# Kernel optimization log

Hardware: AMD Instinct MI355X
Metric: run time of the kernel (lower is better)

## Reference

```python
import jax, jax.numpy as jnp
import numpy as np

B, N, D = 2, 1024, 1024
H = 4
KD = 512          # key_dim = d_model * 0.5
VD = 1024         # value_dim = d_model
DK = KD // H      # 128 head_qk_dim
DV = VD // H      # 256 head_v_dim
LR = 16           # gate_low_rank_dim
GLN = 16.0        # gate_logit_normalizer
EPS = 1e-5


def setup_inputs() -> dict:
    key = jax.random.key(0)
    ks = jax.random.split(key, 10)
    s = 0.02
    return {
        "x": jax.random.normal(ks[0], (B, N, D), jnp.float32),
        "Wq": jax.random.normal(ks[1], (D, KD), jnp.float32) * s,
        "Wk": jax.random.normal(ks[2], (D, KD), jnp.float32) * s,
        "Wv": jax.random.normal(ks[3], (D, VD), jnp.float32) * s,
        "Wg": jax.random.normal(ks[4], (D, VD), jnp.float32) * s,
        "Wgk1": jax.random.normal(ks[5], (D, LR), jnp.float32) * s,
        "Wgk2": jax.random.normal(ks[6], (LR, KD), jnp.float32) * s,
        "bgk2": jax.random.normal(ks[7], (KD,), jnp.float32) * s,
        "Wout": jax.random.normal(ks[8], (VD, D), jnp.float32) * s,
        "rms_w": jnp.ones((DV,), jnp.float32),
    }


def _split_heads(t, h):
    b, n, hd = t.shape
    return t.reshape(b, n, h, hd // h).transpose(0, 2, 1, 3)  # b h n d


def _gla_scan(q, k, v, g):
    # q,k: [b,h,n,dk]; v: [b,h,n,dv]; g: [b,h,n,dk] (log-decay)
    b, h, n, dk = q.shape
    dv = v.shape[-1]
    qT = jnp.moveaxis(q, 2, 0)  # [n,b,h,dk]
    kT = jnp.moveaxis(k, 2, 0)
    vT = jnp.moveaxis(v, 2, 0)
    gT = jnp.moveaxis(g, 2, 0)

    def step(S, inp):
        qt, kt, vt, gt = inp
        # S_t = diag(exp(g_t)) S_{t-1} + k_t v_t^T ; o_t = q_t S_t
        S = S * jnp.exp(gt)[..., None] + kt[..., None] * vt[..., None, :]
        ot = jnp.einsum('bhk,bhkv->bhv', qt, S)
        return S, ot

    S0 = jnp.zeros((b, h, dk, dv), q.dtype)
    _, o = jax.lax.scan(step, S0, (qT, kT, vT, gT))
    return jnp.moveaxis(o, 0, 2)  # [b,h,n,dv]


def reference(x, Wq, Wk, Wv, Wg, Wgk1, Wgk2, bgk2, Wout, rms_w):
    q = _split_heads(x @ Wq, H)
    k = _split_heads(x @ Wk, H)
    v = _split_heads(x @ Wv, H)
    g = jax.nn.log_sigmoid((x @ Wgk1) @ Wgk2 + bgk2) / GLN
    g = jnp.maximum(g, -3.0)  # chunk mode clamp
    g = _split_heads(g, H)
    o = _gla_scan(q, k, v, g)               # [b,h,n,dv]
    o = o.transpose(0, 2, 1, 3)             # [b,n,h,dv]
    # RMSNorm over head_v_dim
    o = o * jax.lax.rsqrt(jnp.mean(o * o, axis=-1, keepdims=True) + EPS) * rms_w
    o = o.reshape(o.shape[0], o.shape[1], VD)
    o = o * jax.nn.silu(x @ Wg)
    return o @ Wout
```

## Files before the change

kernel.cpp:

```cpp
#include <hip/hip_runtime.h>
#include <math.h>


typedef __attribute__((ext_vector_type(4))) float vf4;
typedef __attribute__((ext_vector_type(4))) unsigned int vu4;
typedef __attribute__((ext_vector_type(8))) short short8;

#define DEVI static __device__ __forceinline__
DEVI vf4 vzero() { vf4 x = {0.f, 0.f, 0.f, 0.f}; return x; }

DEVI float bf2f(unsigned int u) {
  union { unsigned int i; float f; } c; c.i = u << 16; return c.f;
}
DEVI unsigned short f2bf(float f) {
  union { float f; unsigned int i; } c; c.f = f;
  unsigned int i = c.i;
  return (unsigned short)((i + 0x7fffu + ((i >> 16) & 1u)) >> 16);
}
DEVI void unpack8(vu4 r, float* f) {
  f[0] = bf2f(r.x & 0xffffu); f[1] = bf2f(r.x >> 16);
  f[2] = bf2f(r.y & 0xffffu); f[3] = bf2f(r.y >> 16);
  f[4] = bf2f(r.z & 0xffffu); f[5] = bf2f(r.z >> 16);
  f[6] = bf2f(r.w & 0xffffu); f[7] = bf2f(r.w >> 16);
}
DEVI vu4 pack8(const float* f) {
  vu4 o;
  o.x = (unsigned int)f2bf(f[0]) | ((unsigned int)f2bf(f[1]) << 16);
  o.y = (unsigned int)f2bf(f[2]) | ((unsigned int)f2bf(f[3]) << 16);
  o.z = (unsigned int)f2bf(f[4]) | ((unsigned int)f2bf(f[5]) << 16);
  o.w = (unsigned int)f2bf(f[6]) | ((unsigned int)f2bf(f[7]) << 16);
  return o;
}

DEVI void gld16(const unsigned short* g, unsigned short* l) {
  __builtin_amdgcn_global_load_lds(
      (const __attribute__((address_space(1))) unsigned int*)g,
      (__attribute__((address_space(3))) unsigned int*)l,
      16, 0, 0);
}

__global__ __launch_bounds__(256)
void prep_k(const float* __restrict__ Wq, const float* __restrict__ Wk,
            const float* __restrict__ Wv, const float* __restrict__ Wg,
            const float* __restrict__ Wo, const float* __restrict__ X,
            unsigned short* __restrict__ wqT, unsigned short* __restrict__ wkT,
            unsigned short* __restrict__ wvT, unsigned short* __restrict__ wgT,
            unsigned short* __restrict__ woT, unsigned short* __restrict__ xb) {
  __shared__ float T[64][65];
  const int ct = blockIdx.x, kt = blockIdx.y;
  const int t = threadIdx.x;
  const int r = t >> 2, s = t & 3;
  if (ct >= 64) {
    const int rt = ct - 64;
    const size_t base = (size_t)(rt * 64 + r) * 1024 + kt * 64 + s * 16;
    float f[16];
    *(vf4*)&f[0]  = *(const vf4*)(X + base);
    *(vf4*)&f[4]  = *(const vf4*)(X + base + 4);
    *(vf4*)&f[8]  = *(const vf4*)(X + base + 8);
    *(vf4*)&f[12] = *(const vf4*)(X + base + 12);
    *(vu4*)(xb + base) = pack8(f);
    *(vu4*)(xb + base + 8) = pack8(f + 8);
    return;
  }
  const float* W; unsigned short* O; int N; int cb;
  if (ct < 8)       { W = Wq; O = wqT; N = 512;  cb = ct; }
  else if (ct < 16) { W = Wk; O = wkT; N = 512;  cb = ct - 8; }
  else if (ct < 32) { W = Wv; O = wvT; N = 1024; cb = ct - 16; }
  else if (ct < 48) { W = Wg; O = wgT; N = 1024; cb = ct - 32; }
  else              { W = Wo; O = woT; N = 1024; cb = ct - 48; }
  const float* src = W + (size_t)(kt * 64 + r) * N + cb * 64 + s * 16;
#pragma unroll
  for (int u = 0; u < 4; ++u) {
    vf4 v4 = *(const vf4*)(src + u * 4);
    T[r][s * 16 + u * 4 + 0] = v4.x;
    T[r][s * 16 + u * 4 + 1] = v4.y;
    T[r][s * 16 + u * 4 + 2] = v4.z;
    T[r][s * 16 + u * 4 + 3] = v4.w;
  }
  __syncthreads();
  unsigned int pk[8];
#pragma unroll
  for (int u = 0; u < 8; ++u) {
    unsigned int lo = f2bf(T[s * 16 + 2 * u][r]);
    unsigned int hi = f2bf(T[s * 16 + 2 * u + 1][r]);
    pk[u] = lo | (hi << 16);
  }
  unsigned short* dst = O + (size_t)(cb * 64 + r) * 1024 + kt * 64 + s * 16;
  *(vu4*)dst = *(vu4*)&pk[0];
  *(vu4*)(dst + 8) = *(vu4*)&pk[4];
}

__global__ __launch_bounds__(256)
void proj_mfma_k(const unsigned short* __restrict__ xb,
                 const unsigned short* __restrict__ wqT, const unsigned short* __restrict__ wkT,
                 const unsigned short* __restrict__ wvT, const unsigned short* __restrict__ wgT,
                 unsigned short* __restrict__ qb, unsigned short* __restrict__ kb,
                 unsigned short* __restrict__ vb, unsigned short* __restrict__ sgb) {
  __shared__ __align__(16) unsigned short As[128 * 64];
  __shared__ __align__(16) unsigned short Bs[128 * 64];
  const int t = threadIdx.x;
  const int m0 = blockIdx.y << 7;
  const int nt = blockIdx.x;
  const unsigned short* WT; int n0; int kind;
  if (nt < 4)       { WT = wqT; n0 = nt << 7;        kind = 0; }
  else if (nt < 8)  { WT = wkT; n0 = (nt - 4) << 7;  kind = 1; }
  else if (nt < 16) { WT = wvT; n0 = (nt - 8) << 7;  kind = 2; }
  else              { WT = wgT; n0 = (nt - 16) << 7; kind = 3; }

  const int w = t >> 6, lane = t & 63;
  const int wm = (w >> 1) << 6, wn = (w & 1) << 6;
  const int qd = lane >> 4, m = lane & 15;
  const int srow = lane >> 3;
  const int scol = ((lane & 7) ^ srow) << 3;

  vf4 acc[4][4];
#pragma unroll
  for (int i = 0; i < 4; ++i)
#pragma unroll
    for (int j = 0; j < 4; ++j) acc[i][j] = vzero();

  for (int k0 = 0; k0 < 1024; k0 += 64) {
    __syncthreads();
#pragma unroll
    for (int cc = 0; cc < 4; ++cc) {
      const int c = (w << 2) + cc;
      const int row = (c << 3) + srow;
      gld16(xb + (size_t)(m0 + row) * 1024 + k0 + scol, (unsigned short*)As + (c << 9));
      gld16(WT + (size_t)(n0 + row) * 1024 + k0 + scol, (unsigned short*)Bs + (c << 9));
    }
    __syncthreads();
#pragma unroll
    for (int ks = 0; ks < 2; ++ks) {
      const int sw = (((ks << 2) + qd) ^ (m & 7)) << 3;
      short8 af[4], bf[4];
#pragma unroll
      for (int i = 0; i < 4; ++i)
        af[i] = *(const short8*)&As[(wm + i * 16 + m) * 64 + sw];
#pragma unroll
      for (int j = 0; j < 4; ++j)
        bf[j] = *(const short8*)&Bs[(wn + j * 16 + m) * 64 + sw];
#pragma unroll
      for (int i = 0; i < 4; ++i)
#pragma unroll
        for (int j = 0; j < 4; ++j)
          acc[i][j] = __builtin_amdgcn_mfma_f32_16x16x32_bf16(af[i], bf[j], acc[i][j], 0, 0, 0);
    }
  }
#pragma unroll
  for (int i = 0; i < 4; ++i) {
#pragma unroll
    for (int j = 0; j < 4; ++j) {
#pragma unroll
      for (int r = 0; r < 4; ++r) {
        const int grow = m0 + wm + i * 16 + qd * 4 + r;
        const int gcol = n0 + wn + j * 16 + m;
        float val = acc[i][j][r];
        if (kind == 0)      qb[(size_t)grow * 512 + gcol] = f2bf(val);
        else if (kind == 1) kb[(size_t)grow * 512 + gcol] = f2bf(val);
        else if (kind == 2) vb[(size_t)grow * 1024 + gcol] = f2bf(val);
        else {
          val = val / (1.f + expf(-val));
          sgb[(size_t)grow * 1024 + gcol] = f2bf(val);
        }
      }
    }
  }
}

__global__ __launch_bounds__(256)
void out_mfma_k(const unsigned short* __restrict__ Ab,
                const unsigned short* __restrict__ woT, float* __restrict__ Y) {
  __shared__ __align__(16) unsigned short As[64 * 64];
  __shared__ __align__(16) unsigned short Bs[128 * 64];
  const int t = threadIdx.x;
  const int m0 = blockIdx.y << 6;
  const int n0 = blockIdx.x << 7;
  const int w = t >> 6, lane = t & 63;
  const int wm = (w >> 1) * 32, wn = (w & 1) * 64;
  const int qd = lane >> 4, m = lane & 15;
  const int srow = lane >> 3;
  const int scol = ((lane & 7) ^ srow) << 3;

  vf4 acc[2][4];
#pragma unroll
  for (int i = 0; i < 2; ++i)
#pragma unroll
    for (int j = 0; j < 4; ++j) acc[i][j] = vzero();

  for (int k0 = 0; k0 < 1024; k0 += 64) {
    __syncthreads();
#pragma unroll
    for (int cc = 0; cc < 2; ++cc) {
      const int c = (w << 1) + cc;
      const int row = (c << 3) + srow;
      gld16(Ab + (size_t)(m0 + row) * 1024 + k0 + scol, (unsigned short*)As + (c << 9));
    }
#pragma unroll
    for (int cc = 0; cc < 4; ++cc) {
      const int c = (w << 2) + cc;
      const int row = (c << 3) + srow;
      gld16(woT + (size_t)(n0 + row) * 1024 + k0 + scol, (unsigned short*)Bs + (c << 9));
    }
    __syncthreads();
#pragma unroll
    for (int ks = 0; ks < 2; ++ks) {
      const int sw = (((ks << 2) + qd) ^ (m & 7)) << 3;
      short8 af[2], bf[4];
#pragma unroll
      for (int i = 0; i < 2; ++i)
        af[i] = *(const short8*)&As[(wm + i * 16 + m) * 64 + sw];
#pragma unroll
      for (int j = 0; j < 4; ++j)
        bf[j] = *(const short8*)&Bs[(wn + j * 16 + m) * 64 + sw];
#pragma unroll
      for (int i = 0; i < 2; ++i)
#pragma unroll
        for (int j = 0; j < 4; ++j)
          acc[i][j] = __builtin_amdgcn_mfma_f32_16x16x32_bf16(af[i], bf[j], acc[i][j], 0, 0, 0);
    }
  }
#pragma unroll
  for (int i = 0; i < 2; ++i)
#pragma unroll
    for (int j = 0; j < 4; ++j)
#pragma unroll
      for (int r = 0; r < 4; ++r) {
        const int grow = m0 + wm + i * 16 + qd * 4 + r;
        const int gcol = n0 + wn + j * 16 + m;
        Y[(size_t)grow * 1024 + gcol] = acc[i][j][r];
      }
}

__global__ __launch_bounds__(64)
void lowrank_k(const float* __restrict__ X, const float* __restrict__ W1,
               float* __restrict__ xl) {
  const int row = blockIdx.x;
  const int t = threadIdx.x;
  float acc[16];
#pragma unroll
  for (int c2 = 0; c2 < 16; ++c2) acc[c2] = 0.f;
  const float* xp = X + (size_t)row * 1024 + t * 16;
  float xv[16];
#pragma unroll
  for (int u = 0; u < 4; ++u)
    *(vf4*)&xv[u * 4] = *(const vf4*)(xp + u * 4);
#pragma unroll
  for (int j = 0; j < 16; ++j) {
    const float* wp = W1 + (size_t)(t * 16 + j) * 16;
    float wv[16];
#pragma unroll
    for (int u = 0; u < 4; ++u)
      *(vf4*)&wv[u * 4] = *(const vf4*)(wp + u * 4);
#pragma unroll
    for (int c2 = 0; c2 < 16; ++c2) acc[c2] = fmaf(xv[j], wv[c2], acc[c2]);
  }
#pragma unroll
  for (int mm = 1; mm < 64; mm <<= 1) {
#pragma unroll
    for (int c2 = 0; c2 < 16; ++c2) acc[c2] += __shfl_xor(acc[c2], mm, 64);
  }
  if (t == 0) {
#pragma unroll
    for (int c2 = 0; c2 < 16; ++c2) xl[(size_t)row * 16 + c2] = acc[c2];
  }
}

__global__ __launch_bounds__(256)
void gate_scan_k(const float* __restrict__ xl, const float* __restrict__ W2,
                 const float* __restrict__ bias,
                 unsigned short* __restrict__ q, unsigned short* __restrict__ k,
                 float* __restrict__ ebtot) {
  const int t = threadIdx.x;
  const int w = t >> 6, lane = t & 63;
  const int wid = blockIdx.x * 4 + w;
  const int kt = wid & 31;
  const int c = (wid >> 5) & 15;
  const int b = wid >> 9;
  const int kbase = kt * 16;
  const size_t rowbase = (size_t)b * 1024 + c * 64;

  const float* xp = xl + (rowbase + lane) * 16;
  float xv[16];
#pragma unroll
  for (int u = 0; u < 4; ++u)
    *(vf4*)&xv[u * 4] = *(const vf4*)(xp + u * 4);

  const size_t a = (rowbase + lane) * 512 + kbase;
  vu4 qr0 = *(const vu4*)(q + a), qr1 = *(const vu4*)(q + a + 8);
  vu4 kr0 = *(const vu4*)(k + a), kr1 = *(const vu4*)(k + a + 8);
  float qf[16], kf[16];
  unpack8(qr0, qf); unpack8(qr1, qf + 8);
  unpack8(kr0, kf); unpack8(kr1, kf + 8);

  float gf[16];
#pragma unroll
  for (int cc = 0; cc < 16; ++cc) {
    const int col = kbase + cc;
    float z = bias[col];
#pragma unroll
    for (int j = 0; j < 16; ++j) z = fmaf(xv[j], W2[j * 512 + col], z);
    float ls = fminf(z, 0.f) - log1pf(expf(-fabsf(z)));
    float g = fmaxf(ls * (1.f / 16.f), -3.f);
#pragma unroll
    for (int d = 1; d < 64; d <<= 1) {
      float up = __shfl_up(g, d, 64);
      if (lane >= d) g += up;
    }
    qf[cc] *= expf(g);
    kf[cc] *= expf(fminf(-g, 80.f));
    gf[cc] = g;
  }
  *(vu4*)(q + a) = pack8(qf);
  *(vu4*)(q + a + 8) = pack8(qf + 8);
  *(vu4*)(k + a) = pack8(kf);
  *(vu4*)(k + a + 8) = pack8(kf + 8);
  if (lane == 63) {
    float* ep = ebtot + ((size_t)b * 16 + c) * 512 + kbase;
#pragma unroll
    for (int cc = 0; cc < 16; ++cc) ep[cc] = expf(gf[cc]);
  }
}

__global__ __launch_bounds__(256)
void intra_kv_k(const unsigned short* __restrict__ q16, const unsigned short* __restrict__ k16,
                const unsigned short* __restrict__ v, float* __restrict__ o,
                unsigned short* __restrict__ ST) {
  __shared__ __align__(16) unsigned short Qs[64 * 136];
  __shared__ __align__(16) unsigned short Ks[64 * 136];
  __shared__ __align__(16) unsigned short Kt[128 * 68];
  __shared__ __align__(16) unsigned short Vt[128 * 68];
  __shared__ __align__(16) unsigned short Asb[64 * 68];
  const int t = threadIdx.x;
  const int vh = blockIdx.x, c = blockIdx.y, bh = blockIdx.z;
  const int b = bh >> 2, h = bh & 3;
  const size_t rowbase = (size_t)b * 1024 + c * 64;

#pragma unroll
  for (int u2 = 0; u2 < 4; ++u2) {
    const int id = t + (u2 << 8);
    const int row = id >> 4, kg = id & 15;
    vu4 rq = *(const vu4*)(q16 + (rowbase + row) * 512 + h * 128 + kg * 8);
    *(vu4*)&Qs[row * 136 + kg * 8] = rq;
    vu4 rk = *(const vu4*)(k16 + (rowbase + row) * 512 + h * 128 + kg * 8);
    *(vu4*)&Ks[row * 136 + kg * 8] = rk;
    const unsigned short* kp = (const unsigned short*)&rk;
#pragma unroll
    for (int u = 0; u < 8; ++u)
      Kt[(kg * 8 + u) * 68 + row] = kp[u];
    vu4 rv = *(const vu4*)(v + (rowbase + row) * 1024 + h * 256 + vh * 128 + kg * 8);
    const unsigned short* vp = (const unsigned short*)&rv;
#pragma unroll
    for (int u = 0; u < 8; ++u)
      Vt[(kg * 8 + u) * 68 + row] = vp[u];
  }
  __syncthreads();

  const int w = t >> 6, lane = t & 63;
  const int qd = lane >> 4, m = lane & 15;

  {
    short8 af[4];
#pragma unroll
    for (int kf = 0; kf < 4; ++kf)
      af[kf] = *(const short8*)&Qs[(w * 16 + m) * 136 + kf * 32 + qd * 8];
    vf4 acc[4];
#pragma unroll
    for (int jt = 0; jt < 4; ++jt) acc[jt] = vzero();
#pragma unroll
    for (int jt = 0; jt < 4; ++jt)
#pragma unroll
      for (int kf = 0; kf < 4; ++kf) {
        short8 bfr = *(const short8*)&Ks[(jt * 16 + m) * 136 + kf * 32 + qd * 8];
        acc[jt] = __builtin_amdgcn_mfma_f32_16x16x32_bf16(af[kf], bfr, acc[jt], 0, 0, 0);
      }
#pragma unroll
    for (int jt = 0; jt < 4; ++jt)
#pragma unroll
      for (int r = 0; r < 4; ++r) {
        const int i = w * 16 + qd * 4 + r;
        const int j = jt * 16 + m;
        Asb[i * 68 + j] = f2bf((j <= i) ? acc[jt][r] : 0.f);
      }
  }
  __syncthreads();

  {
    vf4 acc2[4][2];
#pragma unroll
    for (int mt = 0; mt < 4; ++mt) { acc2[mt][0] = vzero(); acc2[mt][1] = vzero(); }
#pragma unroll
    for (int kf = 0; kf < 2; ++kf) {
      short8 bf0 = *(const short8*)&Vt[(w * 32 + m) * 68 + kf * 32 + qd * 8];
      short8 bf1 = *(const short8*)&Vt[(w * 32 + 16 + m) * 68 + kf * 32 + qd * 8];
#pragma unroll
      for (int mt = 0; mt < 4; ++mt) {
        short8 af = *(const short8*)&Asb[(mt * 16 + m) * 68 + kf * 32 + qd * 8];
        acc2[mt][0] = __builtin_amdgcn_mfma_f32_16x16x32_bf16(af, bf0, acc2[mt][0], 0, 0, 0);
        acc2[mt][1] = __builtin_amdgcn_mfma_f32_16x16x32_bf16(af, bf1, acc2[mt][1], 0, 0, 0);
      }
    }
#pragma unroll
    for (int mt = 0; mt < 4; ++mt)
#pragma unroll
      for (int nt = 0; nt < 2; ++nt)
#pragma unroll
        for (int r = 0; r < 4; ++r) {
          const int i = mt * 16 + qd * 4 + r;
          const int vc = h * 256 + vh * 128 + w * 32 + nt * 16 + m;
          o[(rowbase + i) * 1024 + vc] = acc2[mt][nt][r];
        }
  }

  {
    short8 af3[2][2];
#pragma unroll
    for (int mt = 0; mt < 2; ++mt)
#pragma unroll
      for (int kf = 0; kf < 2; ++kf)
        af3[mt][kf] = *(const short8*)&Vt[(w * 32 + mt * 16 + m) * 68 + kf * 32 + qd * 8];
#pragma unroll
    for (int nt = 0; nt < 8; ++nt) {
      vf4 a0 = vzero(), a1 = vzero();
#pragma unroll
      for (int kf = 0; kf < 2; ++kf) {
        short8 bfr = *(const short8*)&Kt[(nt * 16 + m) * 68 + kf * 32 + qd * 8];
        a0 = __builtin_amdgcn_mfma_f32_16x16x32_bf16(af3[0][kf], bfr, a0, 0, 0, 0);
        a1 = __builtin_amdgcn_mfma_f32_16x16x32_bf16(af3[1][kf], bfr, a1, 0, 0, 0);
      }
      const size_t sbase = (size_t)(bh * 16 + c) * 256 + vh * 128 + w * 32;
#pragma unroll
      for (int r = 0; r < 4; ++r) {
        ST[(sbase + qd * 4 + r) * 128 + nt * 16 + m] = f2bf(a0[r]);
        ST[(sbase + 16 + qd * 4 + r) * 128 + nt * 16 + m] = f2bf(a1[r]);
      }
    }
  }
}

__global__ __launch_bounds__(256)
void state_scan_k(unsigned short* __restrict__ ST, const float* __restrict__ ebtot) {
  const int idx = blockIdx.x * 256 + threadIdx.x;
  const int kg = idx & 15;
  const int vv = (idx >> 4) & 255;
  const int bh = idx >> 12;
  const int b = bh >> 2, h = bh & 3;
  float s[8];
#pragma unroll
  for (int u = 0; u < 8; ++u) s[u] = 0.f;
  for (int c = 0; c < 16; ++c) {
    unsigned short* p = ST + ((size_t)(bh * 16 + c) * 256 + vv) * 128 + kg * 8;
    const float* ep = ebtot + ((size_t)b * 16 + c) * 512 + h * 128 + kg * 8;
    float e[8];
    *(vf4*)&e[0] = *(const vf4*)ep;
    *(vf4*)&e[4] = *(const vf4*)(ep + 4);
    float kv[8];
    unpack8(*(const vu4*)p, kv);
    *(vu4*)p = pack8(s);
#pragma unroll
    for (int u = 0; u < 8; ++u) s[u] = (s[u] + kv[u]) * e[u];
  }
}

__global__ __launch_bounds__(256)
void o_inter_k(const unsigned short* __restrict__ q16, const unsigned short* __restrict__ ST,
               float* __restrict__ o) {
  __shared__ __align__(16) unsigned short Qs[64 * 136];
  __shared__ __align__(16) unsigned short Ss[128 * 136];
  const int t = threadIdx.x;
  const int vt = blockIdx.x, c = blockIdx.y, bh = blockIdx.z;
  const int b = bh >> 2, h = bh & 3;
  const size_t rowbase = (size_t)b * 1024 + c * 64;

#pragma unroll
  for (int u2 = 0; u2 < 4; ++u2) {
    const int id = t + (u2 << 8);
    const int row = id >> 4, kg = id & 15;
    *(vu4*)&Qs[row * 136 + kg * 8] =
        *(const vu4*)(q16 + (rowbase + row) * 512 + h * 128 + kg * 8);
  }
#pragma unroll
  for (int u2 = 0; u2 < 8; ++u2) {
    const int id = t + (u2 << 8);
    const int vrow = id >> 4, kg = id & 15;
    *(vu4*)&Ss[vrow * 136 + kg * 8] =
        *(const vu4*)(ST + ((size_t)(bh * 16 + c) * 256 + vt * 128 + vrow) * 128 + kg * 8);
  }
  __syncthreads();

  const int w = t >> 6, lane = t & 63;
  const int qd = lane >> 4, m = lane & 15;
  short8 af[4];
#pragma unroll
  for (int kf = 0; kf < 4; ++kf)
    af[kf] = *(const short8*)&Qs[(w * 16 + m) * 136 + kf * 32 + qd * 8];
#pragma unroll
  for (int nt = 0; nt < 8; ++nt) {
    vf4 acc = vzero();
#pragma unroll
    for (int kf = 0; kf < 4; ++kf) {
      short8 bfr = *(const short8*)&Ss[(nt * 16 + m) * 136 + kf * 32 + qd * 8];
      acc = __builtin_amdgcn_mfma_f32_16x16x32_bf16(af[kf], bfr, acc, 0, 0, 0);
    }
    float* base = o + (rowbase + w * 16 + qd * 4) * 1024 + h * 256 + vt * 128 + nt * 16 + m;
#pragma unroll
    for (int r = 0; r < 4; ++r)
      base[(size_t)r * 1024] += acc[r];
  }
}

__global__ __launch_bounds__(256)
void norm_gate_k(const float* __restrict__ o, const float* __restrict__ rmsw,
                 const unsigned short* __restrict__ sg,
                 unsigned short* __restrict__ ob) {
  __shared__ float red[4];
  const int grp = blockIdx.x;
  const int row = grp >> 2, h = grp & 3;
  const int t = threadIdx.x;
  const size_t idx = (size_t)row * 1024 + h * 256 + t;
  const float val = o[idx];
  float ss = val * val;
#pragma unroll
  for (int mm = 1; mm < 64; mm <<= 1) ss += __shfl_xor(ss, mm, 64);
  if ((t & 63) == 0) red[t >> 6] = ss;
  __syncthreads();
  const float tot = red[0] + red[1] + red[2] + red[3];
  const float scale = rsqrtf(tot * (1.f / 256.f) + 1e-5f);
  ob[idx] = f2bf(val * scale * rmsw[t] * bf2f((unsigned int)sg[idx]));
}

extern "C" void kernel_launch(void* const* d_in, const int* in_sizes, int n_in,
                              void* d_out, int out_size, void* d_ws, size_t ws_size,
                              hipStream_t stream) {
  const float* x    = (const float*)d_in[0];
  const float* Wq   = (const float*)d_in[1];
  const float* Wk   = (const float*)d_in[2];
  const float* Wv   = (const float*)d_in[3];
  const float* Wg   = (const float*)d_in[4];
  const float* Wgk1 = (const float*)d_in[5];
  const float* Wgk2 = (const float*)d_in[6];
  const float* bgk2 = (const float*)d_in[7];
  const float* Wout = (const float*)d_in[8];
  const float* rmsw = (const float*)d_in[9];

  const size_t MB = 1u << 20;
  char* w = (char*)d_ws;
  unsigned short* qb16   = (unsigned short*)(w);
  unsigned short* kb16   = (unsigned short*)(w + 2 * MB);
  unsigned short* vbuf   = (unsigned short*)(w + 4 * MB);
  unsigned short* sgbuf  = (unsigned short*)(w + 8 * MB);
  float*          obuf   = (float*)(w + 12 * MB);
  char*           sreg   = w + 20 * MB;
  unsigned short* xb     = (unsigned short*)sreg;
  unsigned short* STbuf  = (unsigned short*)sreg;
  unsigned short* obuf_b = (unsigned short*)sreg;
  float*          xlbuf  = (float*)(w + 28 * MB);
  float*          ebbuf  = (float*)(w + 28 * MB + 131072);
  unsigned short* wqT    = (unsigned short*)(w + 29 * MB);
  unsigned short* wkT    = (unsigned short*)(w + 30 * MB);
  unsigned short* wvT    = (unsigned short*)(w + 31 * MB);
  unsigned short* wgT    = (unsigned short*)(w + 33 * MB);
  unsigned short* woT    = (unsigned short*)(w + 35 * MB);

  prep_k<<<dim3(96, 16), 256, 0, stream>>>(Wq, Wk, Wv, Wg, Wout, x,
                                           wqT, wkT, wvT, wgT, woT, xb);
  lowrank_k<<<2048, 64, 0, stream>>>(x, Wgk1, xlbuf);
  proj_mfma_k<<<dim3(24, 16), 256, 0, stream>>>(xb, wqT, wkT, wvT, wgT, qb16, kb16, vbuf, sgbuf);
  gate_scan_k<<<256, 256, 0, stream>>>(xlbuf, Wgk2, bgk2, qb16, kb16, ebbuf);
  intra_kv_k<<<dim3(2, 16, 8), 256, 0, stream>>>(qb16, kb16, vbuf, obuf, STbuf);
  state_scan_k<<<128, 256, 0, stream>>>(STbuf, ebbuf);
  o_inter_k<<<dim3(2, 16, 8), 256, 0, stream>>>(qb16, STbuf, obuf);
  norm_gate_k<<<8192, 256, 0, stream>>>(obuf, rmsw, sgbuf, obuf_b);
  out_mfma_k<<<dim3(8, 32), 256, 0, stream>>>(obuf_b, woT, (float*)d_out);
}
```

Measured before the change: 194.2 us.

## Fuse gate computation into intra/inter chunk kernels and merge prep with lowrank

Removes the separate gate_scan kernel by recomputing the log-decay cumsum inside both the intra-chunk and inter-chunk kernels, applying the decay scaling to q/k in shared memory instead of writing them back to global memory. The lowrank projection is folded into the prep kernel as extra blocks, and norm_gate is vectorised with one wave per head row. This cuts two launches and a global read-modify-write of q and k, at the cost of redundant gate computation in each block and more shared memory (EQ/EK arrays), which may lower occupancy.

```diff
diff --git a/kernel.cpp b/kernel.cpp
--- a/kernel.cpp
+++ b/kernel.cpp
@@ -5,6 +5,7 @@
 typedef __attribute__((ext_vector_type(4))) float vf4;
 typedef __attribute__((ext_vector_type(4))) unsigned int vu4;
 typedef __attribute__((ext_vector_type(8))) short short8;
+typedef __attribute__((ext_vector_type(4))) unsigned short us4;
 
 #define DEVI static __device__ __forceinline__
 DEVI vf4 vzero() { vf4 x = {0.f, 0.f, 0.f, 0.f}; return x; }
@@ -40,15 +41,52 @@
 }
 
 __global__ __launch_bounds__(256)
-void prep_k(const float* __restrict__ Wq, const float* __restrict__ Wk,
-            const float* __restrict__ Wv, const float* __restrict__ Wg,
-            const float* __restrict__ Wo, const float* __restrict__ X,
-            unsigned short* __restrict__ wqT, unsigned short* __restrict__ wkT,
-            unsigned short* __restrict__ wvT, unsigned short* __restrict__ wgT,
-            unsigned short* __restrict__ woT, unsigned short* __restrict__ xb) {
+void prep_lowrank_k(const float* __restrict__ Wq, const float* __restrict__ Wk,
+                    const float* __restrict__ Wv, const float* __restrict__ Wg,
+                    const float* __restrict__ Wo, const float* __restrict__ X,
+                    const float* __restrict__ Wgk1,
+                    unsigned short* __restrict__ wqT, unsigned short* __restrict__ wkT,
+                    unsigned short* __restrict__ wvT, unsigned short* __restrict__ wgT,
+                    unsigned short* __restrict__ woT, unsigned short* __restrict__ xb,
+                    float* __restrict__ xl) {
   __shared__ float T[64][65];
-  const int ct = blockIdx.x, kt = blockIdx.y;
+  const int bid = blockIdx.x;
   const int t = threadIdx.x;
+
+  if (bid >= 1536) {
+    const int w = t >> 6, lane = t & 63;
+    const int row = (bid - 1536) * 4 + w;
+    float acc[16];
+#pragma unroll
+    for (int c2 = 0; c2 < 16; ++c2) acc[c2] = 0.f;
+    const float* xp = X + (size_t)row * 1024 + lane * 16;
+    float xv[16];
+#pragma unroll
+    for (int u = 0; u < 4; ++u)
+      *(vf4*)&xv[u * 4] = *(const vf4*)(xp + u * 4);
+#pragma unroll
+    for (int j = 0; j < 16; ++j) {
+      const float* wp = Wgk1 + (size_t)(lane * 16 + j) * 16;
+      float wv[16];
+#pragma unroll
+      for (int u = 0; u < 4; ++u)
+        *(vf4*)&wv[u * 4] = *(const vf4*)(wp + u * 4);
+#pragma unroll
+      for (int c2 = 0; c2 < 16; ++c2) acc[c2] = fmaf(xv[j], wv[c2], acc[c2]);
+    }
+#pragma unroll
+    for (int mm = 1; mm < 64; mm <<= 1) {
+#pragma unroll
+      for (int c2 = 0; c2 < 16; ++c2) acc[c2] += __shfl_xor(acc[c2], mm, 64);
+    }
+    if (lane == 0) {
+#pragma unroll
+      for (int c2 = 0; c2 < 16; ++c2) xl[(size_t)row * 16 + c2] = acc[c2];
+    }
+    return;
+  }
+
+  const int ct = bid % 96, kt = bid / 96;
   const int r = t >> 2, s = t & 3;
   if (ct >= 64) {
     const int rt = ct - 64;
@@ -168,6 +206,288 @@
 }
 
 __global__ __launch_bounds__(256)
+void intra_gate_k(const float* __restrict__ xl, const float* __restrict__ W2,
+                  const float* __restrict__ bias,
+                  const unsigned short* __restrict__ q16, const unsigned short* __restrict__ k16,
+                  const unsigned short* __restrict__ v, float* __restrict__ o,
+                  unsigned short* __restrict__ ST, float* __restrict__ ebtot) {
+  __shared__ __align__(16) unsigned short Qs[64 * 136];
+  __shared__ __align__(16) unsigned short Ks[64 * 136];
+  __shared__ __align__(16) unsigned short Kt[128 * 68];
+  __shared__ __align__(16) unsigned short Vt[128 * 68];
+  __shared__ __align__(16) unsigned short Asb[64 * 68];
+  __shared__ float EQ[128 * 65];
+  __shared__ float EK[128 * 65];
+  const int t = threadIdx.x;
+  const int vh = blockIdx.x, c = blockIdx.y, bh = blockIdx.z;
+  const int b = bh >> 2, h = bh & 3;
+  const size_t rowbase = (size_t)b * 1024 + c * 64;
+  const int w = t >> 6, lane = t & 63;
+  const int qd = lane >> 4, m = lane & 15;
+
+  {
+    const float* xp = xl + (rowbase + lane) * 16;
+    float xv[16];
+#pragma unroll
+    for (int u = 0; u < 4; ++u)
+      *(vf4*)&xv[u * 4] = *(const vf4*)(xp + u * 4);
+#pragma unroll
+    for (int cc = 0; cc < 32; ++cc) {
+      const int cl = w * 32 + cc;
+      const int col = h * 128 + cl;
+      float z = bias[col];
+#pragma unroll
+      for (int j = 0; j < 16; ++j) z = fmaf(xv[j], W2[j * 512 + col], z);
+      float ls = fminf(z, 0.f) - log1pf(expf(-fabsf(z)));
+      float g = fmaxf(ls * (1.f / 16.f), -3.f);
+#pragma unroll
+      for (int d = 1; d < 64; d <<= 1) {
+        float up = __shfl_up(g, d, 64);
+        if (lane >= d) g += up;
+      }
+      EQ[cl * 65 + lane] = expf(g);
+      EK[cl * 65 + lane] = expf(fminf(-g, 80.f));
+      if (vh == 0 && lane == 63)
+        ebtot[((size_t)b * 16 + c) * 512 + col] = expf(g);
+    }
+  }
+  __syncthreads();
+
+#pragma unroll
+  for (int u2 = 0; u2 < 4; ++u2) {
+    const int id = t + (u2 << 8);
+    const int row = id >> 4, kg = id & 15;
+    vu4 rq = *(const vu4*)(q16 + (rowbase + row) * 512 + h * 128 + kg * 8);
+    vu4 rk = *(const vu4*)(k16 + (rowbase + row) * 512 + h * 128 + kg * 8);
+    float qf[8], kf[8];
+    unpack8(rq, qf); unpack8(rk, kf);
+#pragma unroll
+    for (int u = 0; u < 8; ++u) {
+      qf[u] *= EQ[(kg * 8 + u) * 65 + row];
+      kf[u] *= EK[(kg * 8 + u) * 65 + row];
+    }
+    vu4 pq = pack8(qf), pk4 = pack8(kf);
+    *(vu4*)&Qs[row * 136 + kg * 8] = pq;
+    *(vu4*)&Ks[row * 136 + kg * 8] = pk4;
+    const unsigned short* kp = (const unsigned short*)&pk4;
+#pragma unroll
+    for (int u = 0; u < 8; ++u)
+      Kt[(kg * 8 + u) * 68 + row] = kp[u];
+    vu4 rv = *(const vu4*)(v + (rowbase + row) * 1024 + h * 256 + vh * 128 + kg * 8);
+    const unsigned short* vp = (const unsigned short*)&rv;
+#pragma unroll
+    for (int u = 0; u < 8; ++u)
+      Vt[(kg * 8 + u) * 68 + row] = vp[u];
+  }
+  __syncthreads();
+
+  {
+    short8 af[4];
+#pragma unroll
+    for (int kf = 0; kf < 4; ++kf)
+      af[kf] = *(const short8*)&Qs[(w * 16 + m) * 136 + kf * 32 + qd * 8];
+    vf4 acc[4];
+#pragma unroll
+    for (int jt = 0; jt < 4; ++jt) acc[jt] = vzero();
+#pragma unroll
+    for (int jt = 0; jt < 4; ++jt)
+#pragma unroll
+      for (int kf = 0; kf < 4; ++kf) {
+        short8 bfr = *(const short8*)&Ks[(jt * 16 + m) * 136 + kf * 32 + qd * 8];
+        acc[jt] = __builtin_amdgcn_mfma_f32_16x16x32_bf16(af[kf], bfr, acc[jt], 0, 0, 0);
+      }
+#pragma unroll
+    for (int jt = 0; jt < 4; ++jt)
+#pragma unroll
+      for (int r = 0; r < 4; ++r) {
+        const int i = w * 16 + qd * 4 + r;
+        const int j = jt * 16 + m;
+        Asb[i * 68 + j] = f2bf((j <= i) ? acc[jt][r] : 0.f);
+      }
+  }
+  __syncthreads();
+
+  {
+    vf4 acc2[4][2];
+#pragma unroll
+    for (int mt = 0; mt < 4; ++mt) { acc2[mt][0] = vzero(); acc2[mt][1] = vzero(); }
+#pragma unroll
+    for (int kf = 0; kf < 2; ++kf) {
+      short8 bf0 = *(const short8*)&Vt[(w * 32 + m) * 68 + kf * 32 + qd * 8];
+      short8 bf1 = *(const short8*)&Vt[(w * 32 + 16 + m) * 68 + kf * 32 + qd * 8];
+#pragma unroll
+      for (int mt = 0; mt < 4; ++mt) {
+        short8 af = *(const short8*)&Asb[(mt * 16 + m) * 68 + kf * 32 + qd * 8];
+        acc2[mt][0] = __builtin_amdgcn_mfma_f32_16x16x32_bf16(af, bf0, acc2[mt][0], 0, 0, 0);
+        acc2[mt][1] = __builtin_amdgcn_mfma_f32_16x16x32_bf16(af, bf1, acc2[mt][1], 0, 0, 0);
+      }
+    }
+#pragma unroll
+    for (int mt = 0; mt < 4; ++mt)
+#pragma unroll
+      for (int nt = 0; nt < 2; ++nt)
+#pragma unroll
+        for (int r = 0; r < 4; ++r) {
+          const int i = mt * 16 + qd * 4 + r;
+          const int vc = h * 256 + vh * 128 + w * 32 + nt * 16 + m;
+          o[(rowbase + i) * 1024 + vc] = acc2[mt][nt][r];
+        }
+  }
+
+  {
+    short8 af3[2][2];
+#pragma unroll
+    for (int mt = 0; mt < 2; ++mt)
+#pragma unroll
+      for (int kf = 0; kf < 2; ++kf)
+        af3[mt][kf] = *(const short8*)&Vt[(w * 32 + mt * 16 + m) * 68 + kf * 32 + qd * 8];
+#pragma unroll
+    for (int nt = 0; nt < 8; ++nt) {
+      vf4 a0 = vzero(), a1 = vzero();
+#pragma unroll
+      for (int kf = 0; kf < 2; ++kf) {
+        short8 bfr = *(const short8*)&Kt[(nt * 16 + m) * 68 + kf * 32 + qd * 8];
+        a0 = __builtin_amdgcn_mfma_f32_16x16x32_bf16(af3[0][kf], bfr, a0, 0, 0, 0);
+        a1 = __builtin_amdgcn_mfma_f32_16x16x32_bf16(af3[1][kf], bfr, a1, 0, 0, 0);
+      }
+      const size_t sbase = (size_t)(bh * 16 + c) * 256 + vh * 128 + w * 32;
+#pragma unroll
+      for (int r = 0; r < 4; ++r) {
+        ST[(sbase + qd * 4 + r) * 128 + nt * 16 + m] = f2bf(a0[r]);
+        ST[(sbase + 16 + qd * 4 + r) * 128 + nt * 16 + m] = f2bf(a1[r]);
+      }
+    }
+  }
+}
+
+__global__ __launch_bounds__(256)
+void state_scan_k(unsigned short* __restrict__ ST, const float* __restrict__ ebtot) {
+  const int idx = blockIdx.x * 256 + threadIdx.x;
+  const int kg = idx & 15;
+  const int vv = (idx >> 4) & 255;
+  const int bh = idx >> 12;
+  const int b = bh >> 2, h = bh & 3;
+  float s[8];
+#pragma unroll
+  for (int u = 0; u < 8; ++u) s[u] = 0.f;
+  for (int c = 0; c < 16; ++c) {
+    unsigned short* p = ST + ((size_t)(bh * 16 + c) * 256 + vv) * 128 + kg * 8;
+    const float* ep = ebtot + ((size_t)b * 16 + c) * 512 + h * 128 + kg * 8;
+    float e[8];
+    *(vf4*)&e[0] = *(const vf4*)ep;
+    *(vf4*)&e[4] = *(const vf4*)(ep + 4);
+    float kv[8];
+    unpack8(*(const vu4*)p, kv);
+    *(vu4*)p = pack8(s);
+#pragma unroll
+    for (int u = 0; u < 8; ++u) s[u] = (s[u] + kv[u]) * e[u];
+  }
+}
+
+__global__ __launch_bounds__(256)
+void o_inter_gate_k(const float* __restrict__ xl, const float* __restrict__ W2,
+                    const float* __restrict__ bias,
+                    const unsigned short* __restrict__ q16,
+                    const unsigned short* __restrict__ ST, float* __restrict__ o) {
+  __shared__ __align__(16) unsigned short Qs[64 * 136];
+  __shared__ __align__(16) unsigned short Ss[128 * 136];
+  __shared__ float EQ[128 * 65];
+  const int t = threadIdx.x;
+  const int vt = blockIdx.x, c = blockIdx.y, bh = blockIdx.z;
+  const int b = bh >> 2, h = bh & 3;
+  const size_t rowbase = (size_t)b * 1024 + c * 64;
+  const int w = t >> 6, lane = t & 63;
+  const int qd = lane >> 4, m = lane & 15;
+
+  {
+    const float* xp = xl + (rowbase + lane) * 16;
+    float xv[16];
+#pragma unroll
+    for (int u = 0; u < 4; ++u)
+      *(vf4*)&xv[u * 4] = *(const vf4*)(xp + u * 4);
+#pragma unroll
+    for (int cc = 0; cc < 32; ++cc) {
+      const int cl = w * 32 + cc;
+      const int col = h * 128 + cl;
+      float z = bias[col];
+#pragma unroll
+      for (int j = 0; j < 16; ++j) z = fmaf(xv[j], W2[j * 512 + col], z);
+      float ls = fminf(z, 0.f) - log1pf(expf(-fabsf(z)));
+      float g = fmaxf(ls * (1.f / 16.f), -3.f);
+#pragma unroll
+      for (int d = 1; d < 64; d <<= 1) {
+        float up = __shfl_up(g, d, 64);
+        if (lane >= d) g += up;
+      }
+      EQ[cl * 65 + lane] = expf(g);
+    }
+  }
+  __syncthreads();
+
+#pragma unroll
+  for (int u2 = 0; u2 < 4; ++u2) {
+    const int id = t + (u2 << 8);
+    const int row = id >> 4, kg = id & 15;
+    vu4 rq = *(const vu4*)(q16 + (rowbase + row) * 512 + h * 128 + kg * 8);
+    float qf[8];
+    unpack8(rq, qf);
+#pragma unroll
+    for (int u = 0; u < 8; ++u) qf[u] *= EQ[(kg * 8 + u) * 65 + row];
+    *(vu4*)&Qs[row * 136 + kg * 8] = pack8(qf);
+  }
+#pragma unroll
+  for (int u2 = 0; u2 < 8; ++u2) {
+    const int id = t + (u2 << 8);
+    const int vrow = id >> 4, kg = id & 15;
+    *(vu4*)&Ss[vrow * 136 + kg * 8] =
+        *(const vu4*)(ST + ((size_t)(bh * 16 + c) * 256 + vt * 128 + vrow) * 128 + kg * 8);
+  }
+  __syncthreads();
+
+  short8 af[4];
+#pragma unroll
+  for (int kf = 0; kf < 4; ++kf)
+    af[kf] = *(const short8*)&Qs[(w * 16 + m) * 136 + kf * 32 + qd * 8];
+#pragma unroll
+  for (int nt = 0; nt < 8; ++nt) {
+    vf4 acc = vzero();
+#pragma unroll
+    for (int kf = 0; kf < 4; ++kf) {
+      short8 bfr = *(const short8*)&Ss[(nt * 16 + m) * 136 + kf * 32 + qd * 8];
+      acc = __builtin_amdgcn_mfma_f32_16x16x32_bf16(af[kf], bfr, acc, 0, 0, 0);
+    }
+    float* base = o + (rowbase + w * 16 + qd * 4) * 1024 + h * 256 + vt * 128 + nt * 16 + m;
+#pragma unroll
+    for (int r = 0; r < 4; ++r)
+      base[(size_t)r * 1024] += acc[r];
+  }
+}
+
+__global__ __launch_bounds__(256)
+void norm_gate_k(const float* __restrict__ o, const float* __restrict__ rmsw,
+                 const unsigned short* __restrict__ sg,
+                 unsigned short* __restrict__ ob) {
+  const int t = threadIdx.x;
+  const int w = t >> 6, lane = t & 63;
+  const int grp = blockIdx.x * 4 + w;
+  const int row = grp >> 2, h = grp & 3;
+  const size_t base = (size_t)row * 1024 + h * 256 + lane * 4;
+  vf4 val = *(const vf4*)(o + base);
+  float ss = val.x * val.x + val.y * val.y + val.z * val.z + val.w * val.w;
+#pragma unroll
+  for (int mm = 1; mm < 64; mm <<= 1) ss += __shfl_xor(ss, mm, 64);
+  const float scale = rsqrtf(ss * (1.f / 256.f) + 1e-5f);
+  us4 sgv = *(const us4*)(sg + base);
+  vf4 rw = *(const vf4*)(rmsw + lane * 4);
+  us4 outv;
+  outv.x = f2bf(val.x * scale * rw.x * bf2f((unsigned int)sgv.x));
+  outv.y = f2bf(val.y * scale * rw.y * bf2f((unsigned int)sgv.y));
+  outv.z = f2bf(val.z * scale * rw.z * bf2f((unsigned int)sgv.z));
+  outv.w = f2bf(val.w * scale * rw.w * bf2f((unsigned int)sgv.w));
+  *(us4*)(ob + base) = outv;
+}
+
+__global__ __launch_bounds__(256)
 void out_mfma_k(const unsigned short* __restrict__ Ab,
                 const unsigned short* __restrict__ woT, float* __restrict__ Y) {
   __shared__ __align__(16) unsigned short As[64 * 64];
@@ -229,303 +549,6 @@
         const int gcol = n0 + wn + j * 16 + m;
         Y[(size_t)grow * 1024 + gcol] = acc[i][j][r];
       }
-}
-
-__global__ __launch_bounds__(64)
-void lowrank_k(const float* __restrict__ X, const float* __restrict__ W1,
-               float* __restrict__ xl) {
-  const int row = blockIdx.x;
-  const int t = threadIdx.x;
-  float acc[16];
-#pragma unroll
-  for (int c2 = 0; c2 < 16; ++c2) acc[c2] = 0.f;
-  const float* xp = X + (size_t)row * 1024 + t * 16;
-  float xv[16];
-#pragma unroll
-  for (int u = 0; u < 4; ++u)
-    *(vf4*)&xv[u * 4] = *(const vf4*)(xp + u * 4);
-#pragma unroll
-  for (int j = 0; j < 16; ++j) {
-    const float* wp = W1 + (size_t)(t * 16 + j) * 16;
-    float wv[16];
-#pragma unroll
-    for (int u = 0; u < 4; ++u)
-      *(vf4*)&wv[u * 4] = *(const vf4*)(wp + u * 4);
-#pragma unroll
-    for (int c2 = 0; c2 < 16; ++c2) acc[c2] = fmaf(xv[j], wv[c2], acc[c2]);
-  }
-#pragma unroll
-  for (int mm = 1; mm < 64; mm <<= 1) {
-#pragma unroll
-    for (int c2 = 0; c2 < 16; ++c2) acc[c2] += __shfl_xor(acc[c2], mm, 64);
-  }
-  if (t == 0) {
-#pragma unroll
-    for (int c2 = 0; c2 < 16; ++c2) xl[(size_t)row * 16 + c2] = acc[c2];
-  }
-}
-
-__global__ __launch_bounds__(256)
-void gate_scan_k(const float* __restrict__ xl, const float* __restrict__ W2,
-                 const float* __restrict__ bias,
-                 unsigned short* __restrict__ q, unsigned short* __restrict__ k,
-                 float* __restrict__ ebtot) {
-  const int t = threadIdx.x;
-  const int w = t >> 6, lane = t & 63;
-  const int wid = blockIdx.x * 4 + w;
-  const int kt = wid & 31;
-  const int c = (wid >> 5) & 15;
-  const int b = wid >> 9;
-  const int kbase = kt * 16;
-  const size_t rowbase = (size_t)b * 1024 + c * 64;
-
-  const float* xp = xl + (rowbase + lane) * 16;
-  float xv[16];
-#pragma unroll
-  for (int u = 0; u < 4; ++u)
-    *(vf4*)&xv[u * 4] = *(const vf4*)(xp + u * 4);
-
-  const size_t a = (rowbase + lane) * 512 + kbase;
-  vu4 qr0 = *(const vu4*)(q + a), qr1 = *(const vu4*)(q + a + 8);
-  vu4 kr0 = *(const vu4*)(k + a), kr1 = *(const vu4*)(k + a + 8);
-  float qf[16], kf[16];
-  unpack8(qr0, qf); unpack8(qr1, qf + 8);
-  unpack8(kr0, kf); unpack8(kr1, kf + 8);
-
-  float gf[16];
-#pragma unroll
-  for (int cc = 0; cc < 16; ++cc) {
-    const int col = kbase + cc;
-    float z = bias[col];
-#pragma unroll
-    for (int j = 0; j < 16; ++j) z = fmaf(xv[j], W2[j * 512 + col], z);
-    float ls = fminf(z, 0.f) - log1pf(expf(-fabsf(z)));
-    float g = fmaxf(ls * (1.f / 16.f), -3.f);
-#pragma unroll
-    for (int d = 1; d < 64; d <<= 1) {
-      float up = __shfl_up(g, d, 64);
-      if (lane >= d) g += up;
-    }
-    qf[cc] *= expf(g);
-    kf[cc] *= expf(fminf(-g, 80.f));
-    gf[cc] = g;
-  }
-  *(vu4*)(q + a) = pack8(qf);
-  *(vu4*)(q + a + 8) = pack8(qf + 8);
-  *(vu4*)(k + a) = pack8(kf);
-  *(vu4*)(k + a + 8) = pack8(kf + 8);
-  if (lane == 63) {
-    float* ep = ebtot + ((size_t)b * 16 + c) * 512 + kbase;
-#pragma unroll
-    for (int cc = 0; cc < 16; ++cc) ep[cc] = expf(gf[cc]);
-  }
-}
-
-__global__ __launch_bounds__(256)
-void intra_kv_k(const unsigned short* __restrict__ q16, const unsigned short* __restrict__ k16,
-                const unsigned short* __restrict__ v, float* __restrict__ o,
-                unsigned short* __restrict__ ST) {
-  __shared__ __align__(16) unsigned short Qs[64 * 136];
-  __shared__ __align__(16) unsigned short Ks[64 * 136];
-  __shared__ __align__(16) unsigned short Kt[128 * 68];
-  __shared__ __align__(16) unsigned short Vt[128 * 68];
-  __shared__ __align__(16) unsigned short Asb[64 * 68];
-  const int t = threadIdx.x;
-  const int vh = blockIdx.x, c = blockIdx.y, bh = blockIdx.z;
-  const int b = bh >> 2, h = bh & 3;
-  const size_t rowbase = (size_t)b * 1024 + c * 64;
-
-#pragma unroll
-  for (int u2 = 0; u2 < 4; ++u2) {
-    const int id = t + (u2 << 8);
-    const int row = id >> 4, kg = id & 15;
-    vu4 rq = *(const vu4*)(q16 + (rowbase + row) * 512 + h * 128 + kg * 8);
-    *(vu4*)&Qs[row * 136 + kg * 8] = rq;
-    vu4 rk = *(const vu4*)(k16 + (rowbase + row) * 512 + h * 128 + kg * 8);
-    *(vu4*)&Ks[row * 136 + kg * 8] = rk;
-    const unsigned short* kp = (const unsigned short*)&rk;
-#pragma unroll
-    for (int u = 0; u < 8; ++u)
-      Kt[(kg * 8 + u) * 68 + row] = kp[u];
-    vu4 rv = *(const vu4*)(v + (rowbase + row) * 1024 + h * 256 + vh * 128 + kg * 8);
-    const unsigned short* vp = (const unsigned short*)&rv;
-#pragma unroll
-    for (int u = 0; u < 8; ++u)
-      Vt[(kg * 8 + u) * 68 + row] = vp[u];
-  }
-  __syncthreads();
-
-  const int w = t >> 6, lane = t & 63;
-  const int qd = lane >> 4, m = lane & 15;
-
-  {
-    short8 af[4];
-#pragma unroll
-    for (int kf = 0; kf < 4; ++kf)
-      af[kf] = *(const short8*)&Qs[(w * 16 + m) * 136 + kf * 32 + qd * 8];
-    vf4 acc[4];
-#pragma unroll
-    for (int jt = 0; jt < 4; ++jt) acc[jt] = vzero();
-#pragma unroll
-    for (int jt = 0; jt < 4; ++jt)
-#pragma unroll
-      for (int kf = 0; kf < 4; ++kf) {
-        short8 bfr = *(const short8*)&Ks[(jt * 16 + m) * 136 + kf * 32 + qd * 8];
-        acc[jt] = __builtin_amdgcn_mfma_f32_16x16x32_bf16(af[kf], bfr, acc[jt], 0, 0, 0);
-      }
-#pragma unroll
-    for (int jt = 0; jt < 4; ++jt)
-#pragma unroll
-      for (int r = 0; r < 4; ++r) {
-        const int i = w * 16 + qd * 4 + r;
-        const int j = jt * 16 + m;
-        Asb[i * 68 + j] = f2bf((j <= i) ? acc[jt][r] : 0.f);
-      }
-  }
-  __syncthreads();
-
-  {
-    vf4 acc2[4][2];
-#pragma unroll
-    for (int mt = 0; mt < 4; ++mt) { acc2[mt][0] = vzero(); acc2[mt][1] = vzero(); }
-#pragma unroll
-    for (int kf = 0; kf < 2; ++kf) {
-      short8 bf0 = *(const short8*)&Vt[(w * 32 + m) * 68 + kf * 32 + qd * 8];
-      short8 bf1 = *(const short8*)&Vt[(w * 32 + 16 + m) * 68 + kf * 32 + qd * 8];
-#pragma unroll
-      for (int mt = 0; mt < 4; ++mt) {
-        short8 af = *(const short8*)&Asb[(mt * 16 + m) * 68 + kf * 32 + qd * 8];
-        acc2[mt][0] = __builtin_amdgcn_mfma_f32_16x16x32_bf16(af, bf0, acc2[mt][0], 0, 0, 0);
-        acc2[mt][1] = __builtin_amdgcn_mfma_f32_16x16x32_bf16(af, bf1, acc2[mt][1], 0, 0, 0);
-      }
-    }
-#pragma unroll
-    for (int mt = 0; mt < 4; ++mt)
-#pragma unroll
-      for (int nt = 0; nt < 2; ++nt)
-#pragma unroll
-        for (int r = 0; r < 4; ++r) {
-          const int i = mt * 16 + qd * 4 + r;
-          const int vc = h * 256 + vh * 128 + w * 32 + nt * 16 + m;
-          o[(rowbase + i) * 1024 + vc] = acc2[mt][nt][r];
-        }
-  }
-
-  {
-    short8 af3[2][2];
-#pragma unroll
-    for (int mt = 0; mt < 2; ++mt)
-#pragma unroll
-      for (int kf = 0; kf < 2; ++kf)
-        af3[mt][kf] = *(const short8*)&Vt[(w * 32 + mt * 16 + m) * 68 + kf * 32 + qd * 8];
-#pragma unroll
-    for (int nt = 0; nt < 8; ++nt) {
-      vf4 a0 = vzero(), a1 = vzero();
-#pragma unroll
-      for (int kf = 0; kf < 2; ++kf) {
-        short8 bfr = *(const short8*)&Kt[(nt * 16 + m) * 68 + kf * 32 + qd * 8];
-        a0 = __builtin_amdgcn_mfma_f32_16x16x32_bf16(af3[0][kf], bfr, a0, 0, 0, 0);
-        a1 = __builtin_amdgcn_mfma_f32_16x16x32_bf16(af3[1][kf], bfr, a1, 0, 0, 0);
-      }
-      const size_t sbase = (size_t)(bh * 16 + c) * 256 + vh * 128 + w * 32;
-#pragma unroll
-      for (int r = 0; r < 4; ++r) {
-        ST[(sbase + qd * 4 + r) * 128 + nt * 16 + m] = f2bf(a0[r]);
-        ST[(sbase + 16 + qd * 4 + r) * 128 + nt * 16 + m] = f2bf(a1[r]);
-      }
-    }
-  }
-}
-
-__global__ __launch_bounds__(256)
-void state_scan_k(unsigned short* __restrict__ ST, const float* __restrict__ ebtot) {
-  const int idx = blockIdx.x * 256 + threadIdx.x;
-  const int kg = idx & 15;
-  const int vv = (idx >> 4) & 255;
-  const int bh = idx >> 12;
-  const int b = bh >> 2, h = bh & 3;
-  float s[8];
-#pragma unroll
-  for (int u = 0; u < 8; ++u) s[u] = 0.f;
-  for (int c = 0; c < 16; ++c) {
-    unsigned short* p = ST + ((size_t)(bh * 16 + c) * 256 + vv) * 128 + kg * 8;
-    const float* ep = ebtot + ((size_t)b * 16 + c) * 512 + h * 128 + kg * 8;
-    float e[8];
-    *(vf4*)&e[0] = *(const vf4*)ep;
-    *(vf4*)&e[4] = *(const vf4*)(ep + 4);
-    float kv[8];
-    unpack8(*(const vu4*)p, kv);
-    *(vu4*)p = pack8(s);
-#pragma unroll
-    for (int u = 0; u < 8; ++u) s[u] = (s[u] + kv[u]) * e[u];
-  }
-}
-
-__global__ __launch_bounds__(256)
-void o_inter_k(const unsigned short* __restrict__ q16, const unsigned short* __restrict__ ST,
-               float* __restrict__ o) {
-  __shared__ __align__(16) unsigned short Qs[64 * 136];
-  __shared__ __align__(16) unsigned short Ss[128 * 136];
-  const int t = threadIdx.x;
-  const int vt = blockIdx.x, c = blockIdx.y, bh = blockIdx.z;
-  const int b = bh >> 2, h = bh & 3;
-  const size_t rowbase = (size_t)b * 1024 + c * 64;
-
-#pragma unroll
-  for (int u2 = 0; u2 < 4; ++u2) {
-    const int id = t + (u2 << 8);
-    const int row = id >> 4, kg = id & 15;
-    *(vu4*)&Qs[row * 136 + kg * 8] =
-        *(const vu4*)(q16 + (rowbase + row) * 512 + h * 128 + kg * 8);
-  }
-#pragma unroll
-  for (int u2 = 0; u2 < 8; ++u2) {
-    const int id = t + (u2 << 8);
-    const int vrow = id >> 4, kg = id & 15;
-    *(vu4*)&Ss[vrow * 136 + kg * 8] =
-        *(const vu4*)(ST + ((size_t)(bh * 16 + c) * 256 + vt * 128 + vrow) * 128 + kg * 8);
-  }
-  __syncthreads();
-
-  const int w = t >> 6, lane = t & 63;
-  const int qd = lane >> 4, m = lane & 15;
-  short8 af[4];
-#pragma unroll
-  for (int kf = 0; kf < 4; ++kf)
-    af[kf] = *(const short8*)&Qs[(w * 16 + m) * 136 + kf * 32 + qd * 8];
-#pragma unroll
-  for (int nt = 0; nt < 8; ++nt) {
-    vf4 acc = vzero();
-#pragma unroll
-    for (int kf = 0; kf < 4; ++kf) {
-      short8 bfr = *(const short8*)&Ss[(nt * 16 + m) * 136 + kf * 32 + qd * 8];
-      acc = __builtin_amdgcn_mfma_f32_16x16x32_bf16(af[kf], bfr, acc, 0, 0, 0);
-    }
-    float* base = o + (rowbase + w * 16 + qd * 4) * 1024 + h * 256 + vt * 128 + nt * 16 + m;
-#pragma unroll
-    for (int r = 0; r < 4; ++r)
-      base[(size_t)r * 1024] += acc[r];
-  }
-}
-
-__global__ __launch_bounds__(256)
-void norm_gate_k(const float* __restrict__ o, const float* __restrict__ rmsw,
-                 const unsigned short* __restrict__ sg,
-                 unsigned short* __restrict__ ob) {
-  __shared__ float red[4];
-  const int grp = blockIdx.x;
-  const int row = grp >> 2, h = grp & 3;
-  const int t = threadIdx.x;
-  const size_t idx = (size_t)row * 1024 + h * 256 + t;
-  const float val = o[idx];
-  float ss = val * val;
-#pragma unroll
-  for (int mm = 1; mm < 64; mm <<= 1) ss += __shfl_xor(ss, mm, 64);
-  if ((t & 63) == 0) red[t >> 6] = ss;
-  __syncthreads();
-  const float tot = red[0] + red[1] + red[2] + red[3];
-  const float scale = rsqrtf(tot * (1.f / 256.f) + 1e-5f);
-  ob[idx] = f2bf(val * scale * rmsw[t] * bf2f((unsigned int)sg[idx]));
 }
 
 extern "C" void kernel_launch(void* const* d_in, const int* in_sizes, int n_in,
@@ -561,14 +584,13 @@
   unsigned short* wgT    = (unsigned short*)(w + 33 * MB);
   unsigned short* woT    = (unsigned short*)(w + 35 * MB);
 
-  prep_k<<<dim3(96, 16), 256, 0, stream>>>(Wq, Wk, Wv, Wg, Wout, x,
-                                           wqT, wkT, wvT, wgT, woT, xb);
-  lowrank_k<<<2048, 64, 0, stream>>>(x, Wgk1, xlbuf);
+  prep_lowrank_k<<<2048, 256, 0, stream>>>(Wq, Wk, Wv, Wg, Wout, x, Wgk1,
+                                           wqT, wkT, wvT, wgT, woT, xb, xlbuf);
   proj_mfma_k<<<dim3(24, 16), 256, 0, stream>>>(xb, wqT, wkT, wvT, wgT, qb16, kb16, vbuf, sgbuf);
-  gate_scan_k<<<256, 256, 0, stream>>>(xlbuf, Wgk2, bgk2, qb16, kb16, ebbuf);
-  intra_kv_k<<<dim3(2, 16, 8), 256, 0, stream>>>(qb16, kb16, vbuf, obuf, STbuf);
+  intra_gate_k<<<dim3(2, 16, 8), 256, 0, stream>>>(xlbuf, Wgk2, bgk2, qb16, kb16, vbuf,
+                                                   obuf, STbuf, ebbuf);
   state_scan_k<<<128, 256, 0, stream>>>(STbuf, ebbuf);
-  o_inter_k<<<dim3(2, 16, 8), 256, 0, stream>>>(qb16, STbuf, obuf);
-  norm_gate_k<<<8192, 256, 0, stream>>>(obuf, rmsw, sgbuf, obuf_b);
+  o_inter_gate_k<<<dim3(2, 16, 8), 256, 0, stream>>>(xlbuf, Wgk2, bgk2, qb16, STbuf, obuf);
+  norm_gate_k<<<2048, 256, 0, stream>>>(obuf, rmsw, sgbuf, obuf_b);
   out_mfma_k<<<dim3(8, 32), 256, 0, stream>>>(obuf_b, woT, (float*)d_out);
 }
```

Result: slower. 230.5 us (+18.7%).
